# Optimization experiments

Measured on AMD Instinct MI355X. Metric: run time of the kernel, lower is better.

Reference implementation:

```python
import jax, jax.numpy as jnp
import numpy as np
from jax import lax

S = 8  # down/up-sample factor


def _seg_means(x, z):
    """Directional running means between zero-boundaries along the last axis.

    x: float [..., L] values; z: bool [..., L], True at zero-boundary positions.
    For position t strictly between consecutive boundaries (prev, nxt):
      lr[t] = mean(x[prev:t+1]),  rl[t] = mean(x[t:nxt+1]); else keep x[t].
    """
    L = x.shape[-1]
    ar = jnp.arange(L)
    ax = x.ndim - 1
    # last zero index strictly before t (-1 if none)
    idx = jnp.where(z, ar, -1)
    prev = lax.cummax(idx, axis=ax)
    prev = jnp.concatenate(
        [jnp.full(prev.shape[:-1] + (1,), -1, prev.dtype), prev[..., :-1]], axis=-1)
    # first zero index strictly after t (L if none)
    idx2 = jnp.where(z, ar, L)
    nxt = lax.cummin(idx2, axis=ax, reverse=True)
    nxt = jnp.concatenate(
        [nxt[..., 1:], jnp.full(nxt.shape[:-1] + (1,), L, nxt.dtype)], axis=-1)
    valid = (~z) & (prev >= 0) & (nxt < L)
    # padded cumsum: cs0[..., k] = sum(x[..., :k]), length L+1
    cs0 = jnp.concatenate(
        [jnp.zeros(x.shape[:-1] + (1,), x.dtype), jnp.cumsum(x, axis=-1)], axis=-1)
    prev_c = jnp.clip(prev, 0, L - 1)
    nxt_c = jnp.clip(nxt, 0, L - 1)
    sum_lr = cs0[..., 1:] - jnp.take_along_axis(cs0, prev_c, axis=-1)   # x[prev..t]
    sum_rl = jnp.take_along_axis(cs0, nxt_c + 1, axis=-1) - cs0[..., :-1]  # x[t..nxt]
    cnt_lr = jnp.maximum(ar - prev + 1, 1).astype(x.dtype)
    cnt_rl = jnp.maximum(nxt - ar + 1, 1).astype(x.dtype)
    lr = jnp.where(valid, sum_lr / cnt_lr, x)
    rl = jnp.where(valid, sum_rl / cnt_rl, x)
    return lr, rl


def setup_inputs() -> dict:
    key = jax.random.key(0)
    k0, k1 = jax.random.split(key)
    N, C, H, W = 8, 1, 2048, 2048
    x0 = jax.random.normal(k0, (N, C, H, W), dtype=jnp.float32)
    x1 = jax.random.randint(k1, (N, C, H, W), 0, 8, dtype=jnp.int32)
    return {"x0": x0, "x1": x1}


def reference(x0, x1):
    # nearest-neighbor downsample by 8 (matches F.interpolate scale_factor=1/8, mode='nearest')
    x0d = x0[..., ::S, ::S]
    zd = (x1[..., ::S, ::S] == 0)
    # horizontal pass (along rows)
    xh_lr, xh_rl = _seg_means(x0d, zd)
    # vertical pass (along columns) via transpose
    xv_tb, xv_bt = _seg_means(jnp.swapaxes(x0d, -1, -2), jnp.swapaxes(zd, -1, -2))
    y = xh_lr + xh_rl + jnp.swapaxes(xv_tb, -1, -2) + jnp.swapaxes(xv_bt, -1, -2)
    # nearest-neighbor upsample by 8
    y = jnp.repeat(jnp.repeat(y, S, axis=-2), S, axis=-1)
    return y
```

## Files before the change

### kernel.cpp

```cpp
#include <hip/hip_runtime.h>

#define DS   256
#define FULL 2048
#define NIMG 8

__device__ __forceinline__ float seg_contrib(float x, bool z, int j,
                                             float* s_cs, int* s_prev, int* s_nxt) {
    s_cs[j]   = x;
    s_prev[j] = z ? j : -1;
    s_nxt[j]  = z ? j : DS;
    __syncthreads();
    for (int off = 1; off < DS; off <<= 1) {
        float a = (j >= off)      ? s_cs[j - off]   : 0.0f;
        int   p = (j >= off)      ? s_prev[j - off] : -1;
        int   q = (j + off < DS)  ? s_nxt[j + off]  : DS;
        __syncthreads();
        s_cs[j] += a;
        if (p > s_prev[j]) s_prev[j] = p;
        if (q < s_nxt[j])  s_nxt[j]  = q;
        __syncthreads();
    }
    int prev = (j > 0)      ? s_prev[j - 1] : -1;
    int nxt  = (j < DS - 1) ? s_nxt[j + 1]  : DS;
    bool valid = (!z) && (prev >= 0) && (nxt < DS);
    if (valid) {
        float sum_lr = s_cs[j]   - (prev > 0 ? s_cs[prev - 1] : 0.0f);
        float sum_rl = s_cs[nxt] - (j > 0    ? s_cs[j - 1]    : 0.0f);
        return sum_lr / (float)(j - prev + 1) + sum_rl / (float)(nxt - j + 1);
    }
    return 2.0f * x;
}

__global__ __launch_bounds__(256) void k_horiz(const float* __restrict__ x0,
                                               const int* __restrict__ x1,
                                               float* __restrict__ xd,
                                               unsigned char* __restrict__ zd,
                                               float* __restrict__ yH) {
    __shared__ float s_cs[DS];
    __shared__ int   s_prev[DS];
    __shared__ int   s_nxt[DS];
    int n = blockIdx.x >> 8;
    int i = blockIdx.x & 255;
    int j = threadIdx.x;
    size_t src = (((size_t)n * FULL) + (size_t)i * 8) * FULL + (size_t)j * 8;
    float x = x0[src];
    bool  z = (x1[src] == 0);
    int d = (n << 16) + (i << 8) + j;
    xd[d] = x;
    zd[d] = z ? 1 : 0;
    yH[d] = seg_contrib(x, z, j, s_cs, s_prev, s_nxt);
}

__global__ __launch_bounds__(256) void k_vert(const float* __restrict__ xd,
                                              const unsigned char* __restrict__ zd,
                                              float* __restrict__ yH) {
    __shared__ float s_cs[DS];
    __shared__ int   s_prev[DS];
    __shared__ int   s_nxt[DS];
    int n = blockIdx.x >> 8;
    int c = blockIdx.x & 255;
    int t = threadIdx.x;
    int d = (n << 16) + (t << 8) + c;
    float x = xd[d];
    bool  z = (zd[d] != 0);
    float r = seg_contrib(x, z, t, s_cs, s_prev, s_nxt);
    yH[d] += r;
}

__global__ __launch_bounds__(256) void k_up(const float* __restrict__ yD,
                                            float* __restrict__ out) {
    int gid = blockIdx.x * blockDim.x + threadIdx.x;
    int j4 = gid & 511;
    int r  = gid >> 9;
    int I  = r & 2047;
    int n  = r >> 11;
    int jd = j4 >> 1;
    float v = yD[(n << 16) + ((I >> 3) << 8) + jd];
    ((float4*)out)[gid] = make_float4(v, v, v, v);
}

extern "C" void kernel_launch(void* const* d_in, const int* in_sizes, int n_in,
                              void* d_out, int out_size, void* d_ws, size_t ws_size,
                              hipStream_t stream) {
    const float* x0 = (const float*)d_in[0];
    const int*   x1 = (const int*)d_in[1];
    float* out = (float*)d_out;

    float* xd = (float*)d_ws;
    float* yH = xd + NIMG * DS * DS;
    unsigned char* zd = (unsigned char*)(yH + NIMG * DS * DS);

    dim3 blk(256);
    k_horiz<<<dim3(NIMG * DS), blk, 0, stream>>>(x0, x1, xd, zd, yH);
    k_vert <<<dim3(NIMG * DS), blk, 0, stream>>>(xd, zd, yH);
    k_up   <<<dim3(32768), blk, 0, stream>>>(yH, out);
}
```

Baseline: 50.37 us.

## Replace shared-memory scans with wavefront shuffle scan and ballot boundary masks

Replaces the log-step shared-memory scans for prefix sum, previous-zero and next-zero (each step with two block barriers) with a 64-lane shuffle prefix sum plus per-wave totals, and uses ballot bitmasks with clz/ctz to find segment boundaries. Downsampled x and zero flags are packed into a single float2 workspace array. The upsample kernel now writes two float4 per thread, halving the grid. This cuts barrier and LDS traffic in the scan kernels, at the cost of some serial loops over the 4 waves and a wider intermediate array.

```diff
diff --git a/kernel.cpp b/kernel.cpp
--- a/kernel.cpp
+++ b/kernel.cpp
@@ -4,41 +4,68 @@
 #define FULL 2048
 #define NIMG 8
 
-__device__ __forceinline__ float seg_contrib(float x, bool z, int j,
-                                             float* s_cs, int* s_prev, int* s_nxt) {
-    s_cs[j]   = x;
-    s_prev[j] = z ? j : -1;
-    s_nxt[j]  = z ? j : DS;
+__device__ __forceinline__ float seg_fast(float x, bool z, int j,
+                                          float* s_cs,
+                                          unsigned long long* s_msk,
+                                          float* s_ws) {
+    const int lane = j & 63;
+    const int w    = j >> 6;
+    unsigned long long m = __ballot(z);
+
+    float s = x;
+    #pragma unroll
+    for (int off = 1; off < 64; off <<= 1) {
+        float t = __shfl_up(s, off, 64);
+        if (lane >= off) s += t;
+    }
+    if (lane == 63) s_ws[w]  = s;
+    if (lane == 0)  s_msk[w] = m;
     __syncthreads();
-    for (int off = 1; off < DS; off <<= 1) {
-        float a = (j >= off)      ? s_cs[j - off]   : 0.0f;
-        int   p = (j >= off)      ? s_prev[j - off] : -1;
-        int   q = (j + off < DS)  ? s_nxt[j + off]  : DS;
-        __syncthreads();
-        s_cs[j] += a;
-        if (p > s_prev[j]) s_prev[j] = p;
-        if (q < s_nxt[j])  s_nxt[j]  = q;
-        __syncthreads();
+
+    float pre = 0.f;
+    for (int ww = 0; ww < w; ++ww) pre += s_ws[ww];
+    s += pre;
+    s_cs[j] = s;
+
+    unsigned long long lo = m & ((1ULL << lane) - 1ULL);
+    int prev = -1;
+    if (lo) prev = (w << 6) + 63 - __builtin_clzll(lo);
+    else {
+        for (int ww = w - 1; ww >= 0; --ww) {
+            unsigned long long mm = s_msk[ww];
+            if (mm) { prev = (ww << 6) + 63 - __builtin_clzll(mm); break; }
+        }
     }
-    int prev = (j > 0)      ? s_prev[j - 1] : -1;
-    int nxt  = (j < DS - 1) ? s_nxt[j + 1]  : DS;
+    unsigned long long hi = m & ~((2ULL << lane) - 1ULL);
+    int nxt = DS;
+    if (hi) nxt = (w << 6) + __builtin_ctzll(hi);
+    else {
+        for (int ww = w + 1; ww < 4; ++ww) {
+            unsigned long long mm = s_msk[ww];
+            if (mm) { nxt = (ww << 6) + __builtin_ctzll(mm); break; }
+        }
+    }
+    __syncthreads();
+
     bool valid = (!z) && (prev >= 0) && (nxt < DS);
     if (valid) {
-        float sum_lr = s_cs[j]   - (prev > 0 ? s_cs[prev - 1] : 0.0f);
-        float sum_rl = s_cs[nxt] - (j > 0    ? s_cs[j - 1]    : 0.0f);
-        return sum_lr / (float)(j - prev + 1) + sum_rl / (float)(nxt - j + 1);
+        float cs_j   = s_cs[j];
+        float cs_pm1 = (prev > 0) ? s_cs[prev - 1] : 0.f;
+        float cs_n   = s_cs[nxt];
+        float cs_jm1 = (j > 0) ? s_cs[j - 1] : 0.f;
+        return (cs_j - cs_pm1) / (float)(j - prev + 1)
+             + (cs_n - cs_jm1) / (float)(nxt - j + 1);
     }
-    return 2.0f * x;
+    return 2.f * x;
 }
 
 __global__ __launch_bounds__(256) void k_horiz(const float* __restrict__ x0,
                                                const int* __restrict__ x1,
-                                               float* __restrict__ xd,
-                                               unsigned char* __restrict__ zd,
+                                               float2* __restrict__ xz,
                                                float* __restrict__ yH) {
     __shared__ float s_cs[DS];
-    __shared__ int   s_prev[DS];
-    __shared__ int   s_nxt[DS];
+    __shared__ unsigned long long s_msk[4];
+    __shared__ float s_ws[4];
     int n = blockIdx.x >> 8;
     int i = blockIdx.x & 255;
     int j = threadIdx.x;
@@ -46,37 +73,37 @@
     float x = x0[src];
     bool  z = (x1[src] == 0);
     int d = (n << 16) + (i << 8) + j;
-    xd[d] = x;
-    zd[d] = z ? 1 : 0;
-    yH[d] = seg_contrib(x, z, j, s_cs, s_prev, s_nxt);
+    xz[d] = make_float2(x, z ? 1.f : 0.f);
+    yH[d] = seg_fast(x, z, j, s_cs, s_msk, s_ws);
 }
 
-__global__ __launch_bounds__(256) void k_vert(const float* __restrict__ xd,
-                                              const unsigned char* __restrict__ zd,
+__global__ __launch_bounds__(256) void k_vert(const float2* __restrict__ xz,
                                               float* __restrict__ yH) {
     __shared__ float s_cs[DS];
-    __shared__ int   s_prev[DS];
-    __shared__ int   s_nxt[DS];
+    __shared__ unsigned long long s_msk[4];
+    __shared__ float s_ws[4];
     int n = blockIdx.x >> 8;
     int c = blockIdx.x & 255;
     int t = threadIdx.x;
     int d = (n << 16) + (t << 8) + c;
-    float x = xd[d];
-    bool  z = (zd[d] != 0);
-    float r = seg_contrib(x, z, t, s_cs, s_prev, s_nxt);
+    float2 v = xz[d];
+    float r = seg_fast(v.x, v.y != 0.f, t, s_cs, s_msk, s_ws);
     yH[d] += r;
 }
 
 __global__ __launch_bounds__(256) void k_up(const float* __restrict__ yD,
-                                            float* __restrict__ out) {
-    int gid = blockIdx.x * blockDim.x + threadIdx.x;
-    int j4 = gid & 511;
-    int r  = gid >> 9;
-    int I  = r & 2047;
-    int n  = r >> 11;
-    int jd = j4 >> 1;
+                                            float4* __restrict__ out) {
+    int gid = blockIdx.x * 256 + threadIdx.x;
+    int g2  = gid << 1;
+    int j4  = g2 & 511;
+    int r   = g2 >> 9;
+    int I   = r & 2047;
+    int n   = r >> 11;
+    int jd  = j4 >> 1;
     float v = yD[(n << 16) + ((I >> 3) << 8) + jd];
-    ((float4*)out)[gid] = make_float4(v, v, v, v);
+    float4 vv = make_float4(v, v, v, v);
+    out[g2]     = vv;
+    out[g2 + 1] = vv;
 }
 
 extern "C" void kernel_launch(void* const* d_in, const int* in_sizes, int n_in,
@@ -86,12 +113,11 @@
     const int*   x1 = (const int*)d_in[1];
     float* out = (float*)d_out;
 
-    float* xd = (float*)d_ws;
-    float* yH = xd + NIMG * DS * DS;
-    unsigned char* zd = (unsigned char*)(yH + NIMG * DS * DS);
+    float2* xz = (float2*)d_ws;
+    float*  yH = (float*)(xz + NIMG * DS * DS);
 
     dim3 blk(256);
-    k_horiz<<<dim3(NIMG * DS), blk, 0, stream>>>(x0, x1, xd, zd, yH);
-    k_vert <<<dim3(NIMG * DS), blk, 0, stream>>>(xd, zd, yH);
-    k_up   <<<dim3(32768), blk, 0, stream>>>(yH, out);
+    k_horiz<<<dim3(NIMG * DS), blk, 0, stream>>>(x0, x1, xz, yH);
+    k_vert <<<dim3(NIMG * DS), blk, 0, stream>>>(xz, yH);
+    k_up   <<<dim3(16384), blk, 0, stream>>>(yH, (float4*)out);
 }
```

New measurement: 51.86 us. 1.03x slower.
